# Kernel optimization log

Measured on AMD Instinct MI355X. Metric: run time of the kernel, lower is better.

Reference implementation:

```python
import jax, jax.numpy as jnp
import numpy as np

B, S, D, H, DH, F = 4, 2048, 1024, 16, 64, 4096
EPS = 1e-5


def setup_inputs() -> dict:
    key = jax.random.key(0)
    ks = jax.random.split(key, 8)
    std = 0.02
    return {
        "src": jax.random.normal(ks[0], (B, S, D), dtype=jnp.float32),
        # per-head Q/K/V projections, stacked: [H, D, DH]
        "Wq": jax.random.normal(ks[1], (H, D, DH), dtype=jnp.float32) * std,
        "bq": jnp.zeros((H, DH), dtype=jnp.float32),
        "Wk": jax.random.normal(ks[2], (H, D, DH), dtype=jnp.float32) * std,
        "bk": jnp.zeros((H, DH), dtype=jnp.float32),
        "Wv": jax.random.normal(ks[3], (H, D, DH), dtype=jnp.float32) * std,
        "bv": jnp.zeros((H, DH), dtype=jnp.float32),
        "Wo": jax.random.normal(ks[4], (H * DH, D), dtype=jnp.float32) * std,
        "bo": jnp.zeros((D,), dtype=jnp.float32),
        "ln1_w": jnp.ones((D,), dtype=jnp.float32),
        "ln1_b": jnp.zeros((D,), dtype=jnp.float32),
        "W1": jax.random.normal(ks[5], (D, F), dtype=jnp.float32) * std,
        "b1": jnp.zeros((F,), dtype=jnp.float32),
        "W2": jax.random.normal(ks[6], (F, D), dtype=jnp.float32) * std,
        "b2": jnp.zeros((D,), dtype=jnp.float32),
        "ln2_w": jnp.ones((D,), dtype=jnp.float32),
        "ln2_b": jnp.zeros((D,), dtype=jnp.float32),
    }


def _layernorm(x, w, b):
    m = jnp.mean(x, axis=-1, keepdims=True)
    v = jnp.mean(jnp.square(x - m), axis=-1, keepdims=True)
    return (x - m) * jax.lax.rsqrt(v + EPS) * w + b


def reference(src, Wq, bq, Wk, bk, Wv, bv, Wo, bo, ln1_w, ln1_b, W1, b1, W2, b2, ln2_w, ln2_b):
    # Per-head projections, batched over heads: [B,H,S,DH]
    q = jnp.einsum('bsd,hde->bhse', src, Wq) + bq[None, :, None, :]
    k = jnp.einsum('bsd,hde->bhse', src, Wk) + bk[None, :, None, :]
    v = jnp.einsum('bsd,hde->bhse', src, Wv) + bv[None, :, None, :]
    scale = jnp.asarray(DH, src.dtype) ** 0.5
    scores = jnp.einsum('bhqe,bhke->bhqk', q, k) / scale  # [B,H,S,S]
    attn = jax.nn.softmax(scores, axis=-1)
    ctx = jnp.einsum('bhqk,bhke->bhqe', attn, v)  # [B,H,S,DH]
    # concat heads along feature dim (matches torch.cat over head outputs)
    ctx = ctx.transpose(0, 2, 1, 3).reshape(src.shape[0], src.shape[1], H * DH)
    attn_out = ctx @ Wo + bo
    x = _layernorm(src + attn_out, ln1_w, ln1_b)
    ffn = jax.nn.relu(x @ W1 + b1) @ W2 + b2
    return _layernorm(x + ffn, ln2_w, ln2_b)
```

## Files before the change

kernel.cpp:

```cpp
#include <hip/hip_runtime.h>
#include <stdint.h>


typedef unsigned short u16;
typedef __attribute__((ext_vector_type(8))) short short8;
typedef __attribute__((ext_vector_type(4))) float f32x4;
typedef __attribute__((ext_vector_type(16))) float f32x16;

__device__ __forceinline__ u16 f2bf(float f) {
  union { float f; unsigned u; } v; v.f = f;
  unsigned r = (v.u + 0x7fffu + ((v.u >> 16) & 1u)) >> 16;
  return (u16)r;
}

__device__ __forceinline__ void gl_lds16(const u16* g, u16* l) {
  __builtin_amdgcn_global_load_lds(
      (const __attribute__((address_space(1))) unsigned int*)g,
      (__attribute__((address_space(3))) unsigned int*)l, 16, 0, 0);
}

__device__ __forceinline__ unsigned cvtpk(float lo, float hi) {
  unsigned r;
  asm("v_cvt_pk_bf16_f32 %0, %1, %2" : "=v"(r) : "v"(lo), "v"(hi));
  return r;
}
__device__ __forceinline__ void pl32_swap(unsigned& a, unsigned& b) {
  asm("v_permlane32_swap_b32 %0, %1" : "+v"(a), "+v"(b));
}


__global__ __launch_bounds__(256) void transpose_cast(const float* __restrict__ W,
                                                      u16* __restrict__ WT,
                                                      int K, int N) {
  __shared__ u16 T[64 * 72];
  const int tid = threadIdx.x;
  const long n0 = (long)blockIdx.x * 64, k0 = (long)blockIdx.y * 64;
#pragma unroll
  for (int i = 0; i < 4; i++) {
    int c = tid + i * 256;
    int kr = c >> 4, nc = (c & 15) * 4;
    float4 v = *(const float4*)(W + (k0 + kr) * N + n0 + nc);
    T[(nc + 0) * 72 + kr] = f2bf(v.x);
    T[(nc + 1) * 72 + kr] = f2bf(v.y);
    T[(nc + 2) * 72 + kr] = f2bf(v.z);
    T[(nc + 3) * 72 + kr] = f2bf(v.w);
  }
  __syncthreads();
#pragma unroll
  for (int i = 0; i < 2; i++) {
    int c = tid + i * 256;
    int nr = c >> 3, kc = (c & 7) * 8;
    *(uint4*)(WT + (n0 + nr) * K + k0 + kc) = *(const uint4*)(T + nr * 72 + kc);
  }
}

__global__ __launch_bounds__(256) void transpose_cast_qkv(const float* __restrict__ Wq,
                                                          const float* __restrict__ Wk,
                                                          const float* __restrict__ Wv,
                                                          u16* __restrict__ WT) {
  __shared__ u16 T[64 * 72];
  const int tid = threadIdx.x;
  const int n0 = blockIdx.x * 64, k0 = blockIdx.y * 64;
  const float* W = (n0 < 1024) ? Wq : (n0 < 2048 ? Wk : Wv);
  const int h = (n0 & 1023) >> 6;
#pragma unroll
  for (int i = 0; i < 4; i++) {
    int c = tid + i * 256;
    int kr = c >> 4, ec = (c & 15) * 4;
    float4 v = *(const float4*)(W + ((long)h * 1024 + k0 + kr) * 64 + ec);
    T[(ec + 0) * 72 + kr] = f2bf(v.x);
    T[(ec + 1) * 72 + kr] = f2bf(v.y);
    T[(ec + 2) * 72 + kr] = f2bf(v.z);
    T[(ec + 3) * 72 + kr] = f2bf(v.w);
  }
  __syncthreads();
#pragma unroll
  for (int i = 0; i < 2; i++) {
    int c = tid + i * 256;
    int nr = c >> 3, kc = (c & 7) * 8;
    *(uint4*)(WT + ((long)(n0 + nr)) * 1024 + k0 + kc) = *(const uint4*)(T + nr * 72 + kc);
  }
}

__global__ __launch_bounds__(256) void cast_bf16(const float* __restrict__ x, u16* __restrict__ y) {
  const long i = ((long)blockIdx.x * 256 + threadIdx.x) * 8;
  float4 a = *(const float4*)(x + i);
  float4 b = *(const float4*)(x + i + 4);
  uint4 o;
  o.x = (unsigned)f2bf(a.x) | ((unsigned)f2bf(a.y) << 16);
  o.y = (unsigned)f2bf(a.z) | ((unsigned)f2bf(a.w) << 16);
  o.z = (unsigned)f2bf(b.x) | ((unsigned)f2bf(b.y) << 16);
  o.w = (unsigned)f2bf(b.z) | ((unsigned)f2bf(b.w) << 16);
  *(uint4*)(y + i) = o;
}

__global__ __launch_bounds__(256) void build_bcat(const float* __restrict__ bq,
                                                  const float* __restrict__ bk,
                                                  const float* __restrict__ bv,
                                                  float* __restrict__ bcat) {
  int i = blockIdx.x * 256 + threadIdx.x;
  const float* s = (i < 1024) ? bq : (i < 2048 ? bk : bv);
  bcat[i] = s[i & 1023];
}

#define GEMM_SETUP                                                                 \
  __shared__ __align__(16) u16 As[3][4096];                                        \
  __shared__ __align__(16) u16 Bs[3][4096];                                        \
  const int tid = threadIdx.x;                                                     \
  const int wave = tid >> 6, lane = tid & 63, quad = lane >> 4, l15 = lane & 15;   \
  const int wm = (wave >> 1) * 64, wn = (wave & 1) * 64;                           \
  const int id = blockIdx.x, xcd = id & 7, ii = id >> 3;                           \
  const long m0 = (long)(xcd * 8 + (ii & 7)) * 128, n0 = (long)(ii >> 3) * 128;    \
  const int srow = tid >> 2, sc = (tid & 3) ^ ((srow >> 1) & 3);                   \
  const u16* Ag = A + (m0 + srow) * K + sc * 8;                                    \
  const u16* Bg = B + (n0 + srow) * K + sc * 8;                                    \
  const int cq = quad ^ ((l15 >> 1) & 3);                                          \
  f32x4 acc[4][4] = {};

#define GEMM_STAGE(b, kof)                                                         \
  {                                                                                \
    gl_lds16(Ag + (kof), &As[b][tid * 8]);                                         \
    gl_lds16(Ag + (long)64 * K + (kof), &As[b][tid * 8 + 2048]);                   \
    gl_lds16(Bg + (kof), &Bs[b][tid * 8]);                                         \
    gl_lds16(Bg + (long)64 * K + (kof), &Bs[b][tid * 8 + 2048]);                   \
  }

#define GEMM_KLOOP                                                                 \
  GEMM_STAGE(0, 0)                                                                 \
  GEMM_STAGE(1, 32)                                                                \
  int cur = 0;                                                                     \
  for (int k0 = 0; k0 < K; k0 += 32) {                                             \
    if (k0 + 32 < K) asm volatile("s_waitcnt vmcnt(4)" ::: "memory");              \
    else asm volatile("s_waitcnt vmcnt(0)" ::: "memory");                          \
    __builtin_amdgcn_s_barrier();                                                  \
    if (k0 + 64 < K) {                                                             \
      const int nb = cur == 0 ? 2 : cur - 1;                        \
      GEMM_STAGE(nb, k0 + 64)                                                      \
    }                                                                              \
    short8 af[4], bfr[4];                                                          \
    _Pragma("unroll") for (int t = 0; t < 4; t++)                                  \
        af[t] = *(const short8*)(&As[cur][(wm + t * 16 + l15) * 32 + cq * 8]);     \
    _Pragma("unroll") for (int t = 0; t < 4; t++)                                  \
        bfr[t] = *(const short8*)(&Bs[cur][(wn + t * 16 + l15) * 32 + cq * 8]);    \
    _Pragma("unroll") for (int i = 0; i < 4; i++)                                  \
        _Pragma("unroll") for (int j = 0; j < 4; j++)                              \
            acc[i][j] = __builtin_amdgcn_mfma_f32_16x16x32_bf16(af[i], bfr[j],     \
                                                                acc[i][j], 0, 0, 0); \
    cur = cur == 2 ? 0 : cur + 1;                                                  \
  }

template <int MODE>
__global__ __launch_bounds__(256) void gemm_bt(const u16* __restrict__ A, const u16* __restrict__ B,
                                               const float* __restrict__ bias, void* __restrict__ Cout,
                                               int K, int N) {
  GEMM_SETUP
  float bb[4];
#pragma unroll
  for (int j = 0; j < 4; j++) bb[j] = bias[n0 + wn + j * 16 + l15];
  GEMM_KLOOP
#pragma unroll
  for (int i = 0; i < 4; i++) {
#pragma unroll
    for (int j = 0; j < 4; j++) {
      const long col = n0 + wn + j * 16 + l15;
      const long rowb = m0 + wm + i * 16 + quad * 4;
#pragma unroll
      for (int r = 0; r < 4; r++) {
        float v = acc[i][j][r] + bb[j];
        if (MODE == 2) v = fmaxf(v, 0.f);
        if (MODE == 0)
          ((float*)Cout)[(rowb + r) * N + col] = v;
        else
          ((u16*)Cout)[(rowb + r) * N + col] = f2bf(v);
      }
    }
  }
}

template <int MODE>
__global__ __launch_bounds__(512) void gemm_bt_sk(const u16* __restrict__ A, const u16* __restrict__ B,
                                                  const float* __restrict__ bias, void* __restrict__ Cout,
                                                  int K, int N) {
  __shared__ __align__(16) u16 As[2][2][4096];
  __shared__ __align__(16) u16 Bs[2][2][4096];
  const int tid = threadIdx.x;
  const int wave = tid >> 6, lane = tid & 63, quad = lane >> 4, l15 = lane & 15;
  const int kh = wave >> 2, w4 = wave & 3;
  const int wm = (w4 >> 1) * 64, wn = (w4 & 1) * 64;
  const int id = blockIdx.x, xcd = id & 7, ii = id >> 3;
  const long m0 = (long)(xcd * 8 + (ii & 7)) * 128, n0 = (long)(ii >> 3) * 128;
  const int t = tid & 255;
  const int srow = t >> 2, sc = (t & 3) ^ ((srow >> 1) & 3);
  const int Kh = K >> 1;
  const u16* Ag = A + (m0 + srow) * K + kh * Kh + sc * 8;
  const u16* Bg = B + (n0 + srow) * K + kh * Kh + sc * 8;
  const int cx = (l15 >> 1) & 3;
  f32x4 acc[4][4] = {};
  gl_lds16(Ag, &As[kh][0][t * 8]);
  gl_lds16(Ag + (long)64 * K, &As[kh][0][t * 8 + 2048]);
  gl_lds16(Bg, &Bs[kh][0][t * 8]);
  gl_lds16(Bg + (long)64 * K, &Bs[kh][0][t * 8 + 2048]);
  for (int k0 = 0; k0 < Kh; k0 += 32) {
    __syncthreads();
    const int cur = (k0 >> 5) & 1;
    if (k0 + 32 < Kh) {
      gl_lds16(Ag + k0 + 32, &As[kh][cur ^ 1][t * 8]);
      gl_lds16(Ag + (long)64 * K + k0 + 32, &As[kh][cur ^ 1][t * 8 + 2048]);
      gl_lds16(Bg + k0 + 32, &Bs[kh][cur ^ 1][t * 8]);
      gl_lds16(Bg + (long)64 * K + k0 + 32, &Bs[kh][cur ^ 1][t * 8 + 2048]);
    }
    short8 af[4], bfr[4];
#pragma unroll
    for (int tt = 0; tt < 4; tt++)
      af[tt] = *(const short8*)(&As[kh][cur][(wm + tt * 16 + l15) * 32 + (quad ^ cx) * 8]);
#pragma unroll
    for (int tt = 0; tt < 4; tt++)
      bfr[tt] = *(const short8*)(&Bs[kh][cur][(wn + tt * 16 + l15) * 32 + (quad ^ cx) * 8]);
#pragma unroll
    for (int i = 0; i < 4; i++)
#pragma unroll
      for (int j = 0; j < 4; j++)
        acc[i][j] = __builtin_amdgcn_mfma_f32_16x16x32_bf16(af[i], bfr[j], acc[i][j], 0, 0, 0);
  }
  __syncthreads();
  float* red = (w4 & 2) ? (float*)Bs : (float*)As;
  float* myred = red + (w4 & 1) * 4096 + lane * 4;
  if (kh == 1) {
#pragma unroll
    for (int i = 0; i < 4; i++)
#pragma unroll
      for (int j = 0; j < 4; j++)
        *(f32x4*)(myred + (i * 4 + j) * 256) = acc[i][j];
  }
  __syncthreads();
  if (kh == 0) {
#pragma unroll
    for (int i = 0; i < 4; i++) {
#pragma unroll
      for (int j = 0; j < 4; j++) {
        const f32x4 o = *(const f32x4*)(myred + (i * 4 + j) * 256);
        const long col = n0 + wn + j * 16 + l15;
        const float bb = bias[col];
        const long rowb = m0 + wm + i * 16 + quad * 4;
#pragma unroll
        for (int r = 0; r < 4; r++) {
          float v = acc[i][j][r] + o[r] + bb;
          if (MODE == 2) v = fmaxf(v, 0.f);
          if (MODE == 0)
            ((float*)Cout)[(rowb + r) * N + col] = v;
          else
            ((u16*)Cout)[(rowb + r) * N + col] = f2bf(v);
        }
      }
    }
  }
}

__global__ __launch_bounds__(256) void gemm_qkv(const u16* __restrict__ A, const u16* __restrict__ B,
                                                const float* __restrict__ bias,
                                                u16* __restrict__ QKb, u16* __restrict__ Vt, int K) {
  GEMM_SETUP
  float bb[4];
#pragma unroll
  for (int j = 0; j < 4; j++) bb[j] = bias[n0 + wn + j * 16 + l15];
  GEMM_KLOOP
#pragma unroll
  for (int i = 0; i < 4; i++) {
#pragma unroll
    for (int j = 0; j < 4; j++) {
      const int col0 = (int)n0 + wn + j * 16;
      const int col = col0 + l15;
      const long rowb = m0 + wm + i * 16 + quad * 4;
      if (col0 < 1024) {
#pragma unroll
        for (int r = 0; r < 4; r++)
          QKb[(rowb + r) * 2048 + col] = f2bf((acc[i][j][r] + bb[j]) * 0.1803368801f);
      } else if (col0 < 2048) {
#pragma unroll
        for (int r = 0; r < 4; r++)
          QKb[(rowb + r) * 2048 + col] = f2bf(acc[i][j][r] + bb[j]);
      } else {
        const int ec = col - 2048;
        const int bq = (int)(rowb >> 11), s = (int)(rowb & 2047);
        uint2 p;
        p.x = (unsigned)f2bf(acc[i][j][0] + bb[j]) | ((unsigned)f2bf(acc[i][j][1] + bb[j]) << 16);
        p.y = (unsigned)f2bf(acc[i][j][2] + bb[j]) | ((unsigned)f2bf(acc[i][j][3] + bb[j]) << 16);
        *(uint2*)(Vt + ((long)(bq * 16 + (ec >> 6)) * 64 + (ec & 63)) * 2048 + s) = p;
      }
    }
  }
}


__device__ __forceinline__ void stage_tile(const u16* __restrict__ g, u16* __restrict__ lds, int tid) {
#pragma unroll
  for (int i = 0; i < 2; i++) {
    const int s = i * 256 + tid;
    const int r = s >> 3, cs = s & 7;
    const int c = cs ^ (r & 7);
    gl_lds16(g + (long)r * 2048 + c * 8, lds + s * 8);
  }
}
__device__ __forceinline__ short8 frag(const u16* __restrict__ buf, int row, int chunk) {
  const int slot = row * 8 + (chunk ^ (row & 7));
  return *(const short8*)(buf + slot * 8);
}

__global__ __launch_bounds__(256, 2) void flash_attn(const u16* __restrict__ QKb,
                                                     const u16* __restrict__ Vt,
                                                     u16* __restrict__ ctx) {
  __shared__ __align__(16) u16 Kbuf[2][4096];
  __shared__ __align__(16) u16 Vbuf[2][4096];
  const int tid = threadIdx.x, wave = tid >> 6, lane = tid & 63;
  const int l31 = lane & 31, hi = lane >> 5;
  const int bh = blockIdx.x, b = bh >> 4, h = bh & 15;
  const int qt = blockIdx.y;
  const long qbase = (long)b * 2048 + qt * 256 + wave * 64;
  const u16* Qg = QKb + qbase * 2048 + h * 64;
  const u16* Kg = QKb + ((long)b * 2048) * 2048 + 1024 + h * 64;
  const u16* Vg = Vt + (long)bh * 64 * 2048;

  short8 qf[2][4];
#pragma unroll
  for (int j = 0; j < 2; j++)
#pragma unroll
    for (int ks = 0; ks < 4; ks++)
      qf[j][ks] = *(const short8*)(Qg + (long)(j * 32 + l31) * 2048 + ks * 16 + hi * 8);

  f32x16 O[2][2] = {};
  float rs[2] = {0.f, 0.f};

  stage_tile(Kg, Kbuf[0], tid);
  stage_tile(Vg, Vbuf[0], tid);

  for (int kt = 0; kt < 32; kt++) {
    __syncthreads();
    if (kt < 31) {
      stage_tile(Kg + (long)(kt + 1) * 64 * 2048, Kbuf[(kt + 1) & 1], tid);
      stage_tile(Vg + (kt + 1) * 64, Vbuf[(kt + 1) & 1], tid);
    }
    const u16* Kb = Kbuf[kt & 1];
    const u16* Vb = Vbuf[kt & 1];

#pragma unroll
    for (int m = 0; m < 2; m++) {
      short8 ak[4];
#pragma unroll
      for (int ks = 0; ks < 4; ks++) ak[ks] = frag(Kb, m * 32 + l31, ks * 2 + hi);
      f32x16 S[2] = {};
#pragma unroll
      for (int ks = 0; ks < 4; ks++)
#pragma unroll
        for (int j = 0; j < 2; j++)
          S[j] = __builtin_amdgcn_mfma_f32_32x32x16_bf16(ak[ks], qf[j][ks], S[j], 0, 0, 0);

      short8 pf[2][2];
#pragma unroll
      for (int j = 0; j < 2; j++) {
#pragma unroll
        for (int r = 0; r < 16; r++) S[j][r] = __builtin_amdgcn_exp2f(S[j][r]);
        rs[j] += ((S[j][0] + S[j][1]) + (S[j][2] + S[j][3])) +
                 ((S[j][4] + S[j][5]) + (S[j][6] + S[j][7])) +
                 ((S[j][8] + S[j][9]) + (S[j][10] + S[j][11])) +
                 ((S[j][12] + S[j][13]) + (S[j][14] + S[j][15]));
        unsigned w0 = cvtpk(S[j][0], S[j][1]), w1 = cvtpk(S[j][2], S[j][3]);
        unsigned w2 = cvtpk(S[j][4], S[j][5]), w3 = cvtpk(S[j][6], S[j][7]);
        unsigned w4 = cvtpk(S[j][8], S[j][9]), w5 = cvtpk(S[j][10], S[j][11]);
        unsigned w6 = cvtpk(S[j][12], S[j][13]), w7 = cvtpk(S[j][14], S[j][15]);
        pl32_swap(w2, w0); pl32_swap(w3, w1);
        pl32_swap(w6, w4); pl32_swap(w7, w5);
        union { unsigned u[4]; short8 s8; } f0, f1;
        f0.u[0] = w0; f0.u[1] = w1; f0.u[2] = w2; f0.u[3] = w3;
        f1.u[0] = w4; f1.u[1] = w5; f1.u[2] = w6; f1.u[3] = w7;
        pf[j][0] = f0.s8; pf[j][1] = f1.s8;
      }

#pragma unroll
      for (int et = 0; et < 2; et++) {
        short8 av[2];
#pragma unroll
        for (int ks2 = 0; ks2 < 2; ks2++)
          av[ks2] = frag(Vb, et * 32 + l31, m * 4 + ks2 * 2 + hi);
#pragma unroll
        for (int j = 0; j < 2; j++)
#pragma unroll
          for (int ks2 = 0; ks2 < 2; ks2++)
            O[et][j] = __builtin_amdgcn_mfma_f32_32x32x16_bf16(av[ks2], pf[j][ks2],
                                                               O[et][j], 0, 0, 0);
      }
    }
  }

#pragma unroll
  for (int j = 0; j < 2; j++) rs[j] += __shfl_xor(rs[j], 32);
#pragma unroll
  for (int j = 0; j < 2; j++) {
    const float inv = 1.f / rs[j];
    const long row = qbase + j * 32 + l31;
#pragma unroll
    for (int et = 0; et < 2; et++)
#pragma unroll
      for (int g = 0; g < 4; g++) {
        const int e0 = et * 32 + g * 8 + hi * 4;
        uint2 p;
        p.x = (unsigned)f2bf(O[et][j][g * 4 + 0] * inv) |
              ((unsigned)f2bf(O[et][j][g * 4 + 1] * inv) << 16);
        p.y = (unsigned)f2bf(O[et][j][g * 4 + 2] * inv) |
              ((unsigned)f2bf(O[et][j][g * 4 + 3] * inv) << 16);
        *(uint2*)(ctx + row * 1024 + h * 64 + e0) = p;
      }
  }
}

template <bool WB>
__global__ __launch_bounds__(256) void add_ln(const float* __restrict__ a, const float* __restrict__ c,
                                              const float* __restrict__ w, const float* __restrict__ bias,
                                              float* __restrict__ xout, u16* __restrict__ xbf) {
  const int row = blockIdx.x, tid = threadIdx.x;
  const long off = (long)row * 1024 + tid * 4;
  float4 va = *(const float4*)(a + off);
  float4 vc = *(const float4*)(c + off);
  float4 s = {va.x + vc.x, va.y + vc.y, va.z + vc.z, va.w + vc.w};
  float sum = s.x + s.y + s.z + s.w;
  float sq = s.x * s.x + s.y * s.y + s.z * s.z + s.w * s.w;
#pragma unroll
  for (int o = 32; o > 0; o >>= 1) {
    sum += __shfl_xor(sum, o);
    sq += __shfl_xor(sq, o);
  }
  __shared__ float red[8];
  const int wave = tid >> 6;
  if ((tid & 63) == 0) { red[wave] = sum; red[wave + 4] = sq; }
  __syncthreads();
  sum = red[0] + red[1] + red[2] + red[3];
  sq = red[4] + red[5] + red[6] + red[7];
  const float mean = sum * (1.f / 1024.f);
  const float var = sq * (1.f / 1024.f) - mean * mean;
  const float rstd = rsqrtf(var + 1e-5f);
  float4 vw = *(const float4*)(w + tid * 4);
  float4 vb = *(const float4*)(bias + tid * 4);
  float4 y;
  y.x = (s.x - mean) * rstd * vw.x + vb.x;
  y.y = (s.y - mean) * rstd * vw.y + vb.y;
  y.z = (s.z - mean) * rstd * vw.z + vb.z;
  y.w = (s.w - mean) * rstd * vw.w + vb.w;
  *(float4*)(xout + off) = y;
  if (WB) {
    uint2 o2;
    o2.x = (unsigned)f2bf(y.x) | ((unsigned)f2bf(y.y) << 16);
    o2.y = (unsigned)f2bf(y.z) | ((unsigned)f2bf(y.w) << 16);
    *(uint2*)(xbf + off) = o2;
  }
}

extern "C" void kernel_launch(void* const* d_in, const int* in_sizes, int n_in,
                              void* d_out, int out_size, void* d_ws, size_t ws_size,
                              hipStream_t stream) {
  (void)in_sizes; (void)n_in; (void)out_size; (void)ws_size;
  const float* src = (const float*)d_in[0];
  const float* Wq = (const float*)d_in[1];
  const float* bq = (const float*)d_in[2];
  const float* Wk = (const float*)d_in[3];
  const float* bk = (const float*)d_in[4];
  const float* Wv = (const float*)d_in[5];
  const float* bv = (const float*)d_in[6];
  const float* Wo = (const float*)d_in[7];
  const float* bo = (const float*)d_in[8];
  const float* ln1w = (const float*)d_in[9];
  const float* ln1b = (const float*)d_in[10];
  const float* W1 = (const float*)d_in[11];
  const float* b1 = (const float*)d_in[12];
  const float* W2 = (const float*)d_in[13];
  const float* b2 = (const float*)d_in[14];
  const float* ln2w = (const float*)d_in[15];
  const float* ln2b = (const float*)d_in[16];

  char* ws = (char*)d_ws;
  u16* WqkvT = (u16*)(ws + 0);
  u16* WoT = (u16*)(ws + (6ul << 20));
  u16* W1T = (u16*)(ws + (8ul << 20));
  u16* W2T = (u16*)(ws + (16ul << 20));
  float* bcat = (float*)(ws + (24ul << 20));
  u16* srcb = (u16*)(ws + (25ul << 20));
  u16* QKb = (u16*)(ws + (41ul << 20));
  u16* Vt = (u16*)(ws + (73ul << 20));
  u16* ctxb = (u16*)(ws + (89ul << 20));
  float* x = (float*)(ws + (105ul << 20));
  u16* xb = (u16*)(ws + (137ul << 20));
  u16* hb = (u16*)(ws + (41ul << 20));
  float* out = (float*)d_out;

  transpose_cast_qkv<<<dim3(48, 16), 256, 0, stream>>>(Wq, Wk, Wv, WqkvT);
  transpose_cast<<<dim3(16, 16), 256, 0, stream>>>(Wo, WoT, 1024, 1024);
  transpose_cast<<<dim3(64, 16), 256, 0, stream>>>(W1, W1T, 1024, 4096);
  transpose_cast<<<dim3(16, 64), 256, 0, stream>>>(W2, W2T, 4096, 1024);
  cast_bf16<<<4096, 256, 0, stream>>>(src, srcb);
  build_bcat<<<12, 256, 0, stream>>>(bq, bk, bv, bcat);

  gemm_qkv<<<24 * 64, 256, 0, stream>>>(srcb, WqkvT, bcat, QKb, Vt, 1024);
  flash_attn<<<dim3(64, 8), 256, 0, stream>>>(QKb, Vt, ctxb);
  gemm_bt_sk<0><<<8 * 64, 512, 0, stream>>>(ctxb, WoT, bo, out, 1024, 1024);
  add_ln<true><<<8192, 256, 0, stream>>>(src, out, ln1w, ln1b, x, xb);
  gemm_bt<2><<<32 * 64, 256, 0, stream>>>(xb, W1T, b1, hb, 1024, 4096);
  gemm_bt_sk<0><<<8 * 64, 512, 0, stream>>>(hb, W2T, b2, out, 4096, 1024);
  add_ln<false><<<8192, 256, 0, stream>>>(x, out, ln2w, ln2b, out, nullptr);
}
```

Baseline: 513.1 us.

## Load GEMM A fragments directly from global into registers, double-buffer B in LDS

The A operand tiles are no longer staged through LDS. Each wave now loads its own A fragments straight from global memory into registers, prefetching one k-step ahead, while B keeps an LDS double buffer instead of a triple buffer. This halves LDS use and removes the A-side LDS reads, which could raise occupancy. The cost is redundant global reads of A (both N-waves load the same rows), uncoalesced 16-byte row-strided loads, and a shallower pipeline with a full __syncthreads each iteration.

```diff
diff --git a/kernel.cpp b/kernel.cpp
--- a/kernel.cpp
+++ b/kernel.cpp
@@ -104,49 +104,43 @@
 }
 
 #define GEMM_SETUP                                                                 \
-  __shared__ __align__(16) u16 As[3][4096];                                        \
-  __shared__ __align__(16) u16 Bs[3][4096];                                        \
+  __shared__ __align__(16) u16 Bs[2][4096];                                        \
   const int tid = threadIdx.x;                                                     \
   const int wave = tid >> 6, lane = tid & 63, quad = lane >> 4, l15 = lane & 15;   \
   const int wm = (wave >> 1) * 64, wn = (wave & 1) * 64;                           \
   const int id = blockIdx.x, xcd = id & 7, ii = id >> 3;                           \
   const long m0 = (long)(xcd * 8 + (ii & 7)) * 128, n0 = (long)(ii >> 3) * 128;    \
   const int srow = tid >> 2, sc = (tid & 3) ^ ((srow >> 1) & 3);                   \
-  const u16* Ag = A + (m0 + srow) * K + sc * 8;                                    \
   const u16* Bg = B + (n0 + srow) * K + sc * 8;                                    \
   const int cq = quad ^ ((l15 >> 1) & 3);                                          \
+  const u16* Ap = A + (m0 + wm + l15) * K + quad * 8;                              \
   f32x4 acc[4][4] = {};
 
-#define GEMM_STAGE(b, kof)                                                         \
-  {                                                                                \
-    gl_lds16(Ag + (kof), &As[b][tid * 8]);                                         \
-    gl_lds16(Ag + (long)64 * K + (kof), &As[b][tid * 8 + 2048]);                   \
-    gl_lds16(Bg + (kof), &Bs[b][tid * 8]);                                         \
-    gl_lds16(Bg + (long)64 * K + (kof), &Bs[b][tid * 8 + 2048]);                   \
-  }
-
 #define GEMM_KLOOP                                                                 \
-  GEMM_STAGE(0, 0)                                                                 \
-  GEMM_STAGE(1, 32)                                                                \
-  int cur = 0;                                                                     \
+  gl_lds16(Bg, &Bs[0][tid * 8]);                                                   \
+  gl_lds16(Bg + (long)64 * K, &Bs[0][tid * 8 + 2048]);                             \
+  short8 afc[4], afn[4];                                                           \
+  _Pragma("unroll") for (int t = 0; t < 4; t++)                                    \
+      afc[t] = *(const short8*)(Ap + (long)t * 16 * K);                            \
   for (int k0 = 0; k0 < K; k0 += 32) {                                             \
-    if (k0 + 32 < K) asm volatile("s_waitcnt vmcnt(4)" ::: "memory");              \
-    else asm volatile("s_waitcnt vmcnt(0)" ::: "memory");                          \
-    __builtin_amdgcn_s_barrier();                                                  \
-    if (k0 + 64 < K) {                                                             \
-      const int nb = cur == 0 ? 2 : cur - 1;                        \
-      GEMM_STAGE(nb, k0 + 64)                                                      \
+    __syncthreads();    \
+    const int cur = (k0 >> 5) & 1;                                                 \
+    if (k0 + 32 < K) {                                                             \
+      gl_lds16(Bg + k0 + 32, &Bs[cur ^ 1][tid * 8]);                               \
+      gl_lds16(Bg + (long)64 * K + k0 + 32, &Bs[cur ^ 1][tid * 8 + 2048]);         \
+      _Pragma("unroll") for (int t = 0; t < 4; t++)                                \
+          afn[t] = *(const short8*)(Ap + (long)t * 16 * K + k0 + 32);              \
     }                                                                              \
-    short8 af[4], bfr[4];                                                          \
-    _Pragma("unroll") for (int t = 0; t < 4; t++)                                  \
-        af[t] = *(const short8*)(&As[cur][(wm + t * 16 + l15) * 32 + cq * 8]);     \
+    short8 bfr[4];                                                                 \
     _Pragma("unroll") for (int t = 0; t < 4; t++)                                  \
         bfr[t] = *(const short8*)(&Bs[cur][(wn + t * 16 + l15) * 32 + cq * 8]);    \
     _Pragma("unroll") for (int i = 0; i < 4; i++)                                  \
         _Pragma("unroll") for (int j = 0; j < 4; j++)                              \
-            acc[i][j] = __builtin_amdgcn_mfma_f32_16x16x32_bf16(af[i], bfr[j],     \
+            acc[i][j] = __builtin_amdgcn_mfma_f32_16x16x32_bf16(afc[i], bfr[j],    \
                                                                 acc[i][j], 0, 0, 0); \
-    cur = cur == 2 ? 0 : cur + 1;                                                  \
+    if (k0 + 32 < K) {                                                             \
+      _Pragma("unroll") for (int t = 0; t < 4; t++) afc[t] = afn[t];               \
+    }                                                                              \
   }
 
 template <int MODE>
```

After: 600.8 us. 17.1% more time.
